# Kernel tuning notes

Hardware: AMD Instinct MI355X
Metric: run time of the kernel (lower is better)

The kernel has to match this reference:

```python
import jax, jax.numpy as jnp
import numpy as np

ATTR_LEN = [2, 4, 4, 2, 6]
CUM = np.concatenate(([0], np.cumsum(ATTR_LEN)))  # [0,2,6,10,12,18]
B, S, D, V = 4096, 200, 64, 100000


def setup_inputs() -> dict:
    key = jax.random.key(0)
    ks = jax.random.split(key, 10)
    x = jax.random.randint(ks[0], (B, S), 0, V)
    # one-hot labels per attribute, concatenated -> [B, 18]
    y_parts = []
    for i, al in enumerate(ATTR_LEN):
        lab = jax.random.randint(jax.random.fold_in(ks[1], i), (B,), 0, al)
        y_parts.append(jax.nn.one_hot(lab, al, dtype=jnp.float32))
    y = jnp.concatenate(y_parts, axis=1)
    emb_table = jax.random.normal(ks[2], (V, D), jnp.float32) * 0.02
    emb_table = emb_table.at[0].set(0.0)  # padding_idx=0
    att_w = jax.random.normal(ks[3], (5, D), jnp.float32) * 0.1
    att_b = jax.random.normal(ks[4], (5,), jnp.float32) * 0.1
    W0 = jax.random.normal(ks[5], (ATTR_LEN[0], D), jnp.float32) * 0.1
    W1 = jax.random.normal(ks[6], (ATTR_LEN[1], D), jnp.float32) * 0.1
    W2 = jax.random.normal(ks[7], (ATTR_LEN[2], D), jnp.float32) * 0.1
    W3 = jax.random.normal(ks[8], (ATTR_LEN[3], D), jnp.float32) * 0.1
    W4 = jax.random.normal(ks[9], (ATTR_LEN[4], D), jnp.float32) * 0.1
    return {"x": x, "y": y, "emb_table": emb_table, "att_w": att_w,
            "att_b": att_b, "W0": W0, "W1": W1, "W2": W2, "W3": W3, "W4": W4}


def reference(x, y, emb_table, att_w, att_b, W0, W1, W2, W3, W4):
    embed = emb_table[x]  # [B, S, D] gather (padding row is zero)
    # 5 per-attribute additive tanh-attention heads, batched over k.
    # Softmax over seq axis is independent per head, so stacking is exact.
    att_u = jnp.tanh(jnp.einsum('bsd,kd->bsk', embed, att_w) + att_b)  # [B,S,5]
    score = jax.nn.softmax(att_u, axis=1)                              # [B,S,5]
    user_rep = jnp.einsum('bsd,bsk->bkd', embed, score)                # [B,5,D]
    Ws = [W0, W1, W2, W3, W4]
    # per-task bias-free linear heads, concatenated -> [B, 18]
    W_user = jnp.concatenate([user_rep[:, i] @ Ws[i].T for i in range(5)], axis=1)
    logits = []
    loss = jnp.float32(0.0)
    for i in range(5):
        Wc = W_user[:, CUM[i]:CUM[i + 1]]
        yc = y[:, CUM[i]:CUM[i + 1]]
        # partial_training=False -> ob = ones -> all rows kept;
        # obj = exp(sum(W*y)) / sum_j exp(W_j)  ==  softmax picked at label
        logp = jax.nn.log_softmax(Wc, axis=1)
        loss = loss + (-jnp.sum(logp * yc) / Wc.shape[0])
        logits.append(jax.nn.softmax(Wc, axis=1))
    logit = jnp.concatenate(logits, axis=1)  # [B, 18]
    return logit, loss
```

## Files before the change

### kernel.cpp

```cpp
#include <hip/hip_runtime.h>
#include <math.h>
#include <stdint.h>

#define Bsz 4096
#define Ssz 200
#define Dsz 64
#define NK  5
#define NT  512
#define RST 72
#define TST 232
#define UNIH 14848

typedef _Float16 half_t;
typedef _Float16 h2    __attribute__((ext_vector_type(2)));
typedef _Float16 f16x8 __attribute__((ext_vector_type(8)));
typedef float    f32x4 __attribute__((ext_vector_type(4)));

__device__ inline h2 pk(float a, float b) {
    return __builtin_bit_cast(h2, __builtin_amdgcn_cvt_pkrtz(a, b));
}

__device__ inline float fast_tanh(float x) {
    float e = __expf(-2.0f * fabsf(x));
    float r = (1.0f - e) / (1.0f + e);
    return copysignf(r, x);
}

__global__ void zero_loss_kernel(float* loss) {
    if (threadIdx.x == 0) *loss = 0.0f;
}

__global__ __launch_bounds__(256) void cvt_kernel(const float* __restrict__ src,
                                                  half_t* __restrict__ dst) {
    const size_t i = ((size_t)blockIdx.x * 256 + threadIdx.x) * 8;
    if (i < (size_t)100000 * 64) {
        float4 v0 = *(const float4*)(src + i);
        float4 v1 = *(const float4*)(src + i + 4);
        union { half_t h[8]; uint4 u; } o;
        o.h[0] = (half_t)v0.x; o.h[1] = (half_t)v0.y;
        o.h[2] = (half_t)v0.z; o.h[3] = (half_t)v0.w;
        o.h[4] = (half_t)v1.x; o.h[5] = (half_t)v1.y;
        o.h[6] = (half_t)v1.z; o.h[7] = (half_t)v1.w;
        *(uint4*)(dst + i) = o.u;
    }
}

template <bool F16TAB>
__global__ __launch_bounds__(NT, 8) void tan_kernel(
    const int* __restrict__ x, const float* __restrict__ y,
    const float* __restrict__ emb_table, const half_t* __restrict__ tab16,
    const float* __restrict__ att_w, const float* __restrict__ att_b,
    const float* __restrict__ W0, const float* __restrict__ W1,
    const float* __restrict__ W2, const float* __restrict__ W3,
    const float* __restrict__ W4,
    float* __restrict__ out_logit, float* __restrict__ loss_out)
{
    __shared__ alignas(16) half_t uni[UNIH];
    __shared__ alignas(16) float  ovl[1000];
    __shared__ alignas(16) half_t ascore[NK * 240];
    __shared__ alignas(16) half_t awh[NK * RST];
    __shared__ alignas(16) int    xs[Ssz];
    __shared__ float wu[18];

    half_t* embR = uni;
    half_t* embT = uni;
    float*  att_raw = ovl;

    const int b   = blockIdx.x;
    const int tid = threadIdx.x;
    const int w   = tid >> 6;
    const int l   = tid & 63;
    const int col = l & 15;
    const int kg  = l >> 4;

    if (tid < Ssz) xs[tid] = x[b * Ssz + tid];
    if (tid < 192) {
        const int row = tid / 3, q = tid - row * 3;
        uint4 z = {0u, 0u, 0u, 0u};
        *(uint4*)((char*)embT + row * 464 + 400 + q * 16) = z;
    }
    if (tid >= 256 && tid < 256 + NK * 32) {
        const int t = tid - 256, row = t >> 5, cp = t & 31;
        h2 v = {(half_t)att_w[row * 64 + 2 * cp],
                (half_t)att_w[row * 64 + 2 * cp + 1]};
        *(h2*)(awh + row * RST + 2 * cp) = v;
    }
    __syncthreads();

    if (F16TAB) {
        uint4 g[4];
#pragma unroll
        for (int p = 0; p < 4; ++p) {
            int i = tid + NT * p;
            if (i > 1599) i = 1599;
            const int s = i >> 3, c = i & 7;
            g[p] = *(const uint4*)(tab16 + (size_t)xs[s] * Dsz + c * 8);
        }
#pragma unroll
        for (int p = 0; p < 4; ++p) {
            const int i = tid + NT * p;
            if (p < 3 || i < 1600) {
                const int s = i >> 3, c = i & 7;
                *(uint4*)(embR + s * RST + c * 8) = g[p];
            }
        }
    } else {
        float4 v[7];
#pragma unroll
        for (int p = 0; p < 7; ++p) {
            int i = tid + NT * p;
            if (i > Ssz * 16 - 1) i = Ssz * 16 - 1;
            const int s = i >> 4, c = i & 15;
            v[p] = ((const float4*)(emb_table + (size_t)xs[s] * Dsz))[c];
        }
#pragma unroll
        for (int p = 0; p < 7; ++p) {
            const int i = tid + NT * p;
            if (p < 6 || i < Ssz * 16) {
                const int s = i >> 4, c = i & 15;
                h2 lo = pk(v[p].x, v[p].y);
                h2 hi = pk(v[p].z, v[p].w);
                uint2 u = { __builtin_bit_cast(unsigned, lo),
                            __builtin_bit_cast(unsigned, hi) };
                *(uint2*)(embR + s * RST + c * 4) = u;
            }
        }
    }
    __syncthreads();

    h2 te[4][4];
#pragma unroll
    for (int p = 0; p < 4; ++p) {
        int t = tid + NT * p;
        if (t > 1599) t = 1599;
        const int dp = t & 31, sq = t >> 5;
#pragma unroll
        for (int r = 0; r < 4; ++r)
            te[p][r] = *(const h2*)(embR + (4 * sq + r) * RST + 2 * dp);
    }

    {
        const int brow = (col < 5) ? col : 0;
        const f16x8 bw0 = *(const f16x8*)(awh + brow * RST + kg * 8);
        const f16x8 bw1 = *(const f16x8*)(awh + brow * RST + 32 + kg * 8);
        const float bk = att_b[brow];
        for (int t = w; t < 13; t += 8) {
            const int s  = 16 * t + col;
            const int sr = (s < Ssz) ? s : (Ssz - 1);
            const f16x8 a0 = *(const f16x8*)(embR + sr * RST + kg * 8);
            const f16x8 a1 = *(const f16x8*)(embR + sr * RST + 32 + kg * 8);
            f32x4 acc = {0.f, 0.f, 0.f, 0.f};
            acc = __builtin_amdgcn_mfma_f32_16x16x32_f16(a0, bw0, acc, 0, 0, 0);
            acc = __builtin_amdgcn_mfma_f32_16x16x32_f16(a1, bw1, acc, 0, 0, 0);
            if (col < 5) {
#pragma unroll
                for (int r = 0; r < 4; ++r) {
                    const int srow = 16 * t + 4 * kg + r;
                    if (srow < Ssz)
                        att_raw[col * 200 + srow] = fast_tanh(acc[r] + bk);
                }
            }
        }
    }
    __syncthreads();

#pragma unroll
    for (int p = 0; p < 4; ++p) {
        const int t = tid + NT * p;
        if (t < 1600) {
            const int dp = t & 31, sq = t >> 5;
            h2 lo01 = {te[p][0].x, te[p][1].x}, lo23 = {te[p][2].x, te[p][3].x};
            h2 hi01 = {te[p][0].y, te[p][1].y}, hi23 = {te[p][2].y, te[p][3].y};
            uint2 ulo = { __builtin_bit_cast(unsigned, lo01),
                          __builtin_bit_cast(unsigned, lo23) };
            uint2 uhi = { __builtin_bit_cast(unsigned, hi01),
                          __builtin_bit_cast(unsigned, hi23) };
            *(uint2*)(embT + (2 * dp)     * TST + 4 * sq) = ulo;
            *(uint2*)(embT + (2 * dp + 1) * TST + 4 * sq) = uhi;
        }
    }
    if (w < NK) {
        const int k = w;
        float vals[4];
        float mx = -1e30f;
#pragma unroll
        for (int j = 0; j < 4; ++j) {
            const int s = l + 64 * j;
            vals[j] = (s < Ssz) ? att_raw[k * 200 + s] : -1e30f;
            mx = fmaxf(mx, vals[j]);
        }
#pragma unroll
        for (int m = 32; m >= 1; m >>= 1) mx = fmaxf(mx, __shfl_xor(mx, m));
        float sum = 0.f;
#pragma unroll
        for (int j = 0; j < 4; ++j) {
            vals[j] = __expf(vals[j] - mx);
            sum += vals[j];
        }
#pragma unroll
        for (int m = 32; m >= 1; m >>= 1) sum += __shfl_xor(sum, m);
        const float inv = 1.0f / sum;
#pragma unroll
        for (int j = 0; j < 4; ++j) {
            const int s = l + 64 * j;
            if (s < Ssz)      ascore[k * 240 + s] = (half_t)(vals[j] * inv);
            else if (s < 224) ascore[k * 240 + s] = (half_t)0.0f;
        }
    }
    __syncthreads();

    {
        const int dtile = w & 3, hh = w >> 2;
        const int arow = (col < 5) ? col : 0;
        const int KK0 = hh ? 4 : 0;
        const int NKK = hh ? 3 : 4;
        f32x4 acc = {0.f, 0.f, 0.f, 0.f};
        for (int q = 0; q < NKK; ++q) {
            const int kk = KK0 + q;
            const f16x8 af = *(const f16x8*)(embT + (dtile * 16 + col) * TST
                                             + kk * 32 + kg * 8);
            const f16x8 bf = *(const f16x8*)(ascore + arow * 240 + kk * 32 + kg * 8);
            acc = __builtin_amdgcn_mfma_f32_16x16x32_f16(af, bf, acc, 0, 0, 0);
        }
        float* urp = ovl + hh * 320;
        if (col < 5) {
#pragma unroll
            for (int r = 0; r < 4; ++r)
                urp[col * 64 + dtile * 16 + 4 * kg + r] = acc[r];
        }
    }
    __syncthreads();

    if (tid < NK * Dsz) ovl[640 + tid] = ovl[tid] + ovl[320 + tid];
    __syncthreads();

    for (int j = w; j < 18; j += 8) {
        const float* Wp; int gr, c0;
        if      (j < 2)  { gr = 0; c0 = 0;  Wp = W0; }
        else if (j < 6)  { gr = 1; c0 = 2;  Wp = W1; }
        else if (j < 10) { gr = 2; c0 = 6;  Wp = W2; }
        else if (j < 12) { gr = 3; c0 = 10; Wp = W3; }
        else             { gr = 4; c0 = 12; Wp = W4; }
        float p = ovl[640 + gr * 64 + l] * Wp[(j - c0) * Dsz + l];
#pragma unroll
        for (int m = 32; m >= 1; m >>= 1) p += __shfl_xor(p, m);
        if (l == 0) wu[j] = p;
    }
    __syncthreads();

    if (w == 0) {
        float lossb = 0.f;
        if (l < NK) {
            const int LEN[5] = {2, 4, 4, 2, 6};
            const int C0[5]  = {0, 2, 6, 10, 12};
            const int gidx = l, c0 = C0[gidx], len = LEN[gidx];
            float* op = out_logit + (size_t)b * 18;
            const float* yp = y + (size_t)b * 18;
            float mx = -1e30f;
            for (int j = 0; j < len; ++j) mx = fmaxf(mx, wu[c0 + j]);
            float sum = 0.f;
            for (int j = 0; j < len; ++j) sum += __expf(wu[c0 + j] - mx);
            float inv = 1.0f / sum;
            float lse = mx + __logf(sum);
            for (int j = 0; j < len; ++j) {
                op[c0 + j] = __expf(wu[c0 + j] - mx) * inv;
                lossb += (lse - wu[c0 + j]) * yp[c0 + j];
            }
        }
#pragma unroll
        for (int m = 1; m <= 4; m <<= 1) lossb += __shfl_xor(lossb, m);
        if (l == 0) atomicAdd(loss_out, lossb * (1.0f / Bsz));
    }
}

extern "C" void kernel_launch(void* const* d_in, const int* in_sizes, int n_in,
                              void* d_out, int out_size, void* d_ws, size_t ws_size,
                              hipStream_t stream) {
    const int*   x   = (const int*)d_in[0];
    const float* y   = (const float*)d_in[1];
    const float* emb = (const float*)d_in[2];
    const float* aw  = (const float*)d_in[3];
    const float* ab  = (const float*)d_in[4];
    const float* W0  = (const float*)d_in[5];
    const float* W1  = (const float*)d_in[6];
    const float* W2  = (const float*)d_in[7];
    const float* W3  = (const float*)d_in[8];
    const float* W4  = (const float*)d_in[9];
    float* out  = (float*)d_out;
    float* loss = out + (size_t)Bsz * 18;

    zero_loss_kernel<<<1, 64, 0, stream>>>(loss);

    const size_t need = (size_t)100000 * 64 * sizeof(half_t);
    if (d_ws && ws_size >= need) {
        half_t* tab16 = (half_t*)d_ws;
        cvt_kernel<<<(800000 + 255) / 256, 256, 0, stream>>>(emb, tab16);
        tan_kernel<true><<<Bsz, NT, 0, stream>>>(x, y, emb, tab16, aw, ab,
                                                 W0, W1, W2, W3, W4, out, loss);
    } else {
        tan_kernel<false><<<Bsz, NT, 0, stream>>>(x, y, emb, nullptr, aw, ab,
                                                  W0, W1, W2, W3, W4, out, loss);
    }
}
```

Before: 157.4 us.

## Process two batch rows per block, prefetching the second row's embedding gather

The fp16-table kernel now handles two batch rows per workgroup. It issues the gathers for both rows up front so the second row's global loads overlap the first row's compute, and folds the first row's softmax/loss head into the second iteration. Custom barriers (lgkmcnt wait plus s_barrier) replace __syncthreads, and the extra partial-sum reduction pass is fused into the head dot product. The cost is more registers held for the prefetched data, half as many blocks, and less grid parallelism.

```diff
diff --git a/kernel.cpp b/kernel.cpp
--- a/kernel.cpp
+++ b/kernel.cpp
@@ -24,6 +24,12 @@
     float e = __expf(-2.0f * fabsf(x));
     float r = (1.0f - e) / (1.0f + e);
     return copysignf(r, x);
+}
+
+__device__ inline void phase_bar() {
+    asm volatile("s_waitcnt lgkmcnt(0)" ::: "memory");
+    __builtin_amdgcn_s_barrier();
+    __builtin_amdgcn_sched_barrier(0);
 }
 
 __global__ void zero_loss_kernel(float* loss) {
@@ -45,10 +51,236 @@
     }
 }
 
-template <bool F16TAB>
-__global__ __launch_bounds__(NT, 8) void tan_kernel(
+__device__ inline void head_phase(int b, const float* wu, const float* __restrict__ y,
+                                  float* __restrict__ out_logit, float& lossacc, int l) {
+    if (l < NK) {
+        const int LEN[5] = {2, 4, 4, 2, 6};
+        const int C0[5]  = {0, 2, 6, 10, 12};
+        const int g = l, c0 = C0[g], len = LEN[g];
+        float* op = out_logit + (size_t)b * 18;
+        const float* yp = y + (size_t)b * 18;
+        float mx = -1e30f;
+        for (int j = 0; j < len; ++j) mx = fmaxf(mx, wu[c0 + j]);
+        float sum = 0.f;
+        for (int j = 0; j < len; ++j) sum += __expf(wu[c0 + j] - mx);
+        float inv = 1.0f / sum;
+        float lse = mx + __logf(sum);
+        for (int j = 0; j < len; ++j) {
+            op[c0 + j] = __expf(wu[c0 + j] - mx) * inv;
+            lossacc += (lse - wu[c0 + j]) * yp[c0 + j];
+        }
+    }
+}
+
+__global__ __launch_bounds__(NT, 8) void tan2_kernel(
     const int* __restrict__ x, const float* __restrict__ y,
-    const float* __restrict__ emb_table, const half_t* __restrict__ tab16,
+    const half_t* __restrict__ tab16,
+    const float* __restrict__ att_w, const float* __restrict__ att_b,
+    const float* __restrict__ W0, const float* __restrict__ W1,
+    const float* __restrict__ W2, const float* __restrict__ W3,
+    const float* __restrict__ W4,
+    float* __restrict__ out_logit, float* __restrict__ loss_out)
+{
+    __shared__ alignas(16) half_t uni[UNIH];
+    __shared__ alignas(16) float  ovl[1000];
+    __shared__ alignas(16) half_t ascore[NK * 240];
+    __shared__ alignas(16) half_t awh[NK * RST];
+    __shared__ float wu[18];
+
+    half_t* embR = uni;
+    half_t* embT = uni;
+    float*  att_raw = ovl;
+
+    const int blk = blockIdx.x;
+    const int b0  = 2 * blk, b1 = 2 * blk + 1;
+    const int tid = threadIdx.x;
+    const int w   = tid >> 6;
+    const int l   = tid & 63;
+    const int col = l & 15;
+    const int kg  = l >> 4;
+
+    float lossacc = 0.f;
+
+    {
+        uint4 z = {0u, 0u, 0u, 0u};
+        if (tid < 200)
+            *(uint4*)((char*)uni + tid * 144 + 128) = z;
+        else if (tid < 256)
+            *(uint4*)((char*)uni + 28800 + (tid - 200) * 16) = z;
+    }
+    if (tid >= 256 && tid < 256 + NK * 32) {
+        const int t = tid - 256, row = t >> 5, cp = t & 31;
+        h2 v = {(half_t)att_w[row * 64 + 2 * cp],
+                (half_t)att_w[row * 64 + 2 * cp + 1]};
+        *(h2*)(awh + row * RST + 2 * cp) = v;
+    }
+    uint4 ga[4], gb[4];
+#pragma unroll
+    for (int p = 0; p < 4; ++p) {
+        int i = tid + NT * p;
+        if (i > 1599) i = 1599;
+        const int s = i >> 3, c = i & 7;
+        ga[p] = *(const uint4*)(tab16 + (size_t)x[b0 * Ssz + s] * Dsz + c * 8);
+    }
+#pragma unroll
+    for (int p = 0; p < 4; ++p) {
+        int i = tid + NT * p;
+        if (i > 1599) i = 1599;
+        const int s = i >> 3, c = i & 7;
+        gb[p] = *(const uint4*)(tab16 + (size_t)x[b1 * Ssz + s] * Dsz + c * 8);
+    }
+#pragma unroll
+    for (int p = 0; p < 4; ++p) {
+        const int i = tid + NT * p;
+        if (p < 3 || i < 1600) {
+            const int s = i >> 3, c = i & 7;
+            *(uint4*)(embR + s * RST + c * 8) = ga[p];
+        }
+    }
+    phase_bar();
+
+    h2 te[4][4];
+#pragma unroll 1
+    for (int bb = 0; bb < 2; ++bb) {
+#pragma unroll
+        for (int p = 0; p < 4; ++p) {
+            int t = tid + NT * p;
+            if (t > 1599) t = 1599;
+            const int dp = t & 31, sq = t >> 5;
+#pragma unroll
+            for (int r = 0; r < 4; ++r)
+                te[p][r] = *(const h2*)(embR + (4 * sq + r) * RST + 2 * dp);
+        }
+        {
+            const int brow = (col < 5) ? col : 0;
+            const f16x8 bw0 = *(const f16x8*)(awh + brow * RST + kg * 8);
+            const f16x8 bw1 = *(const f16x8*)(awh + brow * RST + 32 + kg * 8);
+            const float bk = att_b[brow];
+            for (int t = w; t < 13; t += 8) {
+                const int s  = 16 * t + col;
+                const int sr = (s < Ssz) ? s : (Ssz - 1);
+                const f16x8 a0 = *(const f16x8*)(embR + sr * RST + kg * 8);
+                const f16x8 a1 = *(const f16x8*)(embR + sr * RST + 32 + kg * 8);
+                f32x4 acc = {0.f, 0.f, 0.f, 0.f};
+                acc = __builtin_amdgcn_mfma_f32_16x16x32_f16(a0, bw0, acc, 0, 0, 0);
+                acc = __builtin_amdgcn_mfma_f32_16x16x32_f16(a1, bw1, acc, 0, 0, 0);
+                if (col < 5) {
+#pragma unroll
+                    for (int r = 0; r < 4; ++r) {
+                        const int srow = 16 * t + 4 * kg + r;
+                        if (srow < Ssz)
+                            att_raw[col * 200 + srow] = fast_tanh(acc[r] + bk);
+                    }
+                }
+            }
+        }
+        if (bb == 1 && w == 0) head_phase(b0, wu, y, out_logit, lossacc, l);
+        phase_bar();
+
+#pragma unroll
+        for (int p = 0; p < 4; ++p) {
+            const int t = tid + NT * p;
+            if (t < 1600) {
+                const int dp = t & 31, sq = t >> 5;
+                h2 lo01 = {te[p][0].x, te[p][1].x}, lo23 = {te[p][2].x, te[p][3].x};
+                h2 hi01 = {te[p][0].y, te[p][1].y}, hi23 = {te[p][2].y, te[p][3].y};
+                uint2 ulo = { __builtin_bit_cast(unsigned, lo01),
+                              __builtin_bit_cast(unsigned, lo23) };
+                uint2 uhi = { __builtin_bit_cast(unsigned, hi01),
+                              __builtin_bit_cast(unsigned, hi23) };
+                *(uint2*)(embT + (2 * dp)     * TST + 4 * sq) = ulo;
+                *(uint2*)(embT + (2 * dp + 1) * TST + 4 * sq) = uhi;
+            }
+        }
+        if (w < NK) {
+            const int k = w;
+            float vals[4];
+            float mx = -1e30f;
+#pragma unroll
+            for (int j = 0; j < 4; ++j) {
+                const int s = l + 64 * j;
+                vals[j] = (s < Ssz) ? att_raw[k * 200 + s] : -1e30f;
+                mx = fmaxf(mx, vals[j]);
+            }
+#pragma unroll
+            for (int m = 32; m >= 1; m >>= 1) mx = fmaxf(mx, __shfl_xor(mx, m));
+            float sum = 0.f;
+#pragma unroll
+            for (int j = 0; j < 4; ++j) {
+                vals[j] = __expf(vals[j] - mx);
+                sum += vals[j];
+            }
+#pragma unroll
+            for (int m = 32; m >= 1; m >>= 1) sum += __shfl_xor(sum, m);
+            const float inv = 1.0f / sum;
+#pragma unroll
+            for (int j = 0; j < 4; ++j) {
+                const int s = l + 64 * j;
+                if (s < Ssz)      ascore[k * 240 + s] = (half_t)(vals[j] * inv);
+                else if (s < 224) ascore[k * 240 + s] = (half_t)0.0f;
+            }
+        }
+        phase_bar();
+
+        {
+            const int dtile = w & 3, hh = w >> 2;
+            const int arow = (col < 5) ? col : 0;
+            const int KK0 = hh ? 4 : 0;
+            const int NKK = hh ? 3 : 4;
+            f32x4 acc = {0.f, 0.f, 0.f, 0.f};
+            for (int q = 0; q < NKK; ++q) {
+                const int kk = KK0 + q;
+                const f16x8 af = *(const f16x8*)(embT + (dtile * 16 + col) * TST
+                                                 + kk * 32 + kg * 8);
+                const f16x8 bf = *(const f16x8*)(ascore + arow * 240 + kk * 32 + kg * 8);
+                acc = __builtin_amdgcn_mfma_f32_16x16x32_f16(af, bf, acc, 0, 0, 0);
+            }
+            float* urp = ovl + hh * 320;
+            if (col < 5) {
+#pragma unroll
+                for (int r = 0; r < 4; ++r)
+                    urp[col * 64 + dtile * 16 + 4 * kg + r] = acc[r];
+            }
+        }
+        phase_bar();
+
+        if (bb == 0) {
+#pragma unroll
+            for (int p = 0; p < 4; ++p) {
+                const int i = tid + NT * p;
+                if (p < 3 || i < 1600) {
+                    const int s = i >> 3, c = i & 7;
+                    *(uint4*)(embR + s * RST + c * 8) = gb[p];
+                }
+            }
+        }
+        for (int j = w; j < 18; j += 8) {
+            const float* Wp; int gr, c0;
+            if      (j < 2)  { gr = 0; c0 = 0;  Wp = W0; }
+            else if (j < 6)  { gr = 1; c0 = 2;  Wp = W1; }
+            else if (j < 10) { gr = 2; c0 = 6;  Wp = W2; }
+            else if (j < 12) { gr = 3; c0 = 10; Wp = W3; }
+            else             { gr = 4; c0 = 12; Wp = W4; }
+            float p = (ovl[gr * 64 + l] + ovl[320 + gr * 64 + l])
+                      * Wp[(j - c0) * Dsz + l];
+#pragma unroll
+            for (int m = 32; m >= 1; m >>= 1) p += __shfl_xor(p, m);
+            if (l == 0) wu[j] = p;
+        }
+        phase_bar();
+    }
+
+    if (w == 0) {
+        head_phase(b1, wu, y, out_logit, lossacc, l);
+#pragma unroll
+        for (int m = 1; m <= 4; m <<= 1) lossacc += __shfl_xor(lossacc, m);
+        if (l == 0) atomicAdd(loss_out, lossacc * (1.0f / Bsz));
+    }
+}
+
+__global__ __launch_bounds__(NT, 8) void tan1_kernel(
+    const int* __restrict__ x, const float* __restrict__ y,
+    const float* __restrict__ emb_table,
     const float* __restrict__ att_w, const float* __restrict__ att_b,
     const float* __restrict__ W0, const float* __restrict__ W1,
     const float* __restrict__ W2, const float* __restrict__ W3,
@@ -74,37 +306,26 @@
     const int kg  = l >> 4;
 
     if (tid < Ssz) xs[tid] = x[b * Ssz + tid];
-    if (tid < 192) {
-        const int row = tid / 3, q = tid - row * 3;
+    {
         uint4 z = {0u, 0u, 0u, 0u};
-        *(uint4*)((char*)embT + row * 464 + 400 + q * 16) = z;
-    }
-    if (tid >= 256 && tid < 256 + NK * 32) {
-        const int t = tid - 256, row = t >> 5, cp = t & 31;
-        h2 v = {(half_t)att_w[row * 64 + 2 * cp],
-                (half_t)att_w[row * 64 + 2 * cp + 1]};
-        *(h2*)(awh + row * RST + 2 * cp) = v;
+        if (tid >= 200 && tid < 400)
+            *(uint4*)((char*)uni + (tid - 200) * 144 + 128) = z;
+        else if (tid >= 400 && tid < 456)
+            *(uint4*)((char*)uni + 28800 + (tid - 400) * 16) = z;
+    }
+    if (tid >= 456 && tid < 456 + 40) {
+        const int t = tid - 456, row = t >> 3, cp = t & 7;
+        h2 v0 = {(half_t)att_w[row * 64 + 8 * cp + 0], (half_t)att_w[row * 64 + 8 * cp + 1]};
+        h2 v1 = {(half_t)att_w[row * 64 + 8 * cp + 2], (half_t)att_w[row * 64 + 8 * cp + 3]};
+        h2 v2 = {(half_t)att_w[row * 64 + 8 * cp + 4], (half_t)att_w[row * 64 + 8 * cp + 5]};
+        h2 v3 = {(half_t)att_w[row * 64 + 8 * cp + 6], (half_t)att_w[row * 64 + 8 * cp + 7]};
+        *(h2*)(awh + row * RST + 8 * cp + 0) = v0;
+        *(h2*)(awh + row * RST + 8 * cp + 2) = v1;
+        *(h2*)(awh + row * RST + 8 * cp + 4) = v2;
+        *(h2*)(awh + row * RST + 8 * cp + 6) = v3;
     }
     __syncthreads();
-
-    if (F16TAB) {
-        uint4 g[4];
-#pragma unroll
-        for (int p = 0; p < 4; ++p) {
-            int i = tid + NT * p;
-            if (i > 1599) i = 1599;
-            const int s = i >> 3, c = i & 7;
-            g[p] = *(const uint4*)(tab16 + (size_t)xs[s] * Dsz + c * 8);
-        }
-#pragma unroll
-        for (int p = 0; p < 4; ++p) {
-            const int i = tid + NT * p;
-            if (p < 3 || i < 1600) {
-                const int s = i >> 3, c = i & 7;
-                *(uint4*)(embR + s * RST + c * 8) = g[p];
-            }
-        }
-    } else {
+    {
         float4 v[7];
 #pragma unroll
         for (int p = 0; p < 7; ++p) {
@@ -127,7 +348,6 @@
         }
     }
     __syncthreads();
-
     h2 te[4][4];
 #pragma unroll
     for (int p = 0; p < 4; ++p) {
@@ -138,7 +358,6 @@
         for (int r = 0; r < 4; ++r)
             te[p][r] = *(const h2*)(embR + (4 * sq + r) * RST + 2 * dp);
     }
-
     {
         const int brow = (col < 5) ? col : 0;
         const f16x8 bw0 = *(const f16x8*)(awh + brow * RST + kg * 8);
@@ -163,7 +382,6 @@
         }
     }
     __syncthreads();
-
 #pragma unroll
     for (int p = 0; p < 4; ++p) {
         const int t = tid + NT * p;
@@ -208,7 +426,6 @@
         }
     }
     __syncthreads();
-
     {
         const int dtile = w & 3, hh = w >> 2;
         const int arow = (col < 5) ? col : 0;
@@ -230,10 +447,6 @@
         }
     }
     __syncthreads();
-
-    if (tid < NK * Dsz) ovl[640 + tid] = ovl[tid] + ovl[320 + tid];
-    __syncthreads();
-
     for (int j = w; j < 18; j += 8) {
         const float* Wp; int gr, c0;
         if      (j < 2)  { gr = 0; c0 = 0;  Wp = W0; }
@@ -241,32 +454,15 @@
         else if (j < 10) { gr = 2; c0 = 6;  Wp = W2; }
         else if (j < 12) { gr = 3; c0 = 10; Wp = W3; }
         else             { gr = 4; c0 = 12; Wp = W4; }
-        float p = ovl[640 + gr * 64 + l] * Wp[(j - c0) * Dsz + l];
+        float p = (ovl[gr * 64 + l] + ovl[320 + gr * 64 + l]) * Wp[(j - c0) * Dsz + l];
 #pragma unroll
         for (int m = 32; m >= 1; m >>= 1) p += __shfl_xor(p, m);
         if (l == 0) wu[j] = p;
     }
     __syncthreads();
-
     if (w == 0) {
         float lossb = 0.f;
-        if (l < NK) {
-            const int LEN[5] = {2, 4, 4, 2, 6};
-            const int C0[5]  = {0, 2, 6, 10, 12};
-            const int gidx = l, c0 = C0[gidx], len = LEN[gidx];
-            float* op = out_logit + (size_t)b * 18;
-            const float* yp = y + (size_t)b * 18;
-            float mx = -1e30f;
-            for (int j = 0; j < len; ++j) mx = fmaxf(mx, wu[c0 + j]);
-            float sum = 0.f;
-            for (int j = 0; j < len; ++j) sum += __expf(wu[c0 + j] - mx);
-            float inv = 1.0f / sum;
-            float lse = mx + __logf(sum);
-            for (int j = 0; j < len; ++j) {
-                op[c0 + j] = __expf(wu[c0 + j] - mx) * inv;
-                lossb += (lse - wu[c0 + j]) * yp[c0 + j];
-            }
-        }
+        head_phase(b, wu, y, out_logit, lossb, l);
 #pragma unroll
         for (int m = 1; m <= 4; m <<= 1) lossb += __shfl_xor(lossb, m);
         if (l == 0) atomicAdd(loss_out, lossb * (1.0f / Bsz));
@@ -294,11 +490,11 @@
     const size_t need = (size_t)100000 * 64 * sizeof(half_t);
     if (d_ws && ws_size >= need) {
         half_t* tab16 = (half_t*)d_ws;
-        cvt_kernel<<<(800000 + 255) / 256, 256, 0, stream>>>(emb, tab16);
-        tan_kernel<true><<<Bsz, NT, 0, stream>>>(x, y, emb, tab16, aw, ab,
-                                                 W0, W1, W2, W3, W4, out, loss);
+        cvt_kernel<<<3125, 256, 0, stream>>>(emb, tab16);
+        tan2_kernel<<<Bsz / 2, NT, 0, stream>>>(x, y, tab16, aw, ab,
+                                                W0, W1, W2, W3, W4, out, loss);
     } else {
-        tan_kernel<false><<<Bsz, NT, 0, stream>>>(x, y, emb, nullptr, aw, ab,
-                                                  W0, W1, W2, W3, W4, out, loss);
-    }
-}
+        tan1_kernel<<<Bsz, NT, 0, stream>>>(x, y, emb, aw, ab,
+                                            W0, W1, W2, W3, W4, out, loss);
+    }
+}
```

After: 171.7 us. 1.09x slower.
